# Kernel optimization log

Measured on AMD Instinct MI355X. Metric: run time of the kernel, lower is better.

The kernel has to match this reference:

```python
import jax, jax.numpy as jnp
import numpy as np

B, T_ENC, IN_SIZE = 512, 256, 32
HID, N_LAYERS, OUT_SIZE, PRED_W = 256, 2, 1, 30


def _lstm_layer(x, h0, c0, W_ih, W_hh, b_ih, b_hh):
    """x: [B,T,D]; PyTorch gate order i,f,g,o. Returns (ys [B,T,H], h, c)."""
    pre = jnp.einsum('btd,gd->btg', x, W_ih) + b_ih  # precompute input gates [B,T,4H]
    def step(carry, p):
        h, c = carry
        gates = p + h @ W_hh.T + b_hh
        i, f, g, o = jnp.split(gates, 4, axis=-1)
        c = jax.nn.sigmoid(f) * c + jax.nn.sigmoid(i) * jnp.tanh(g)
        h = jax.nn.sigmoid(o) * jnp.tanh(c)
        return (h, c), h
    (h, c), ys = jax.lax.scan(step, (h0, c0), jnp.swapaxes(pre, 0, 1))
    return jnp.swapaxes(ys, 0, 1), h, c


def _lstm_stack(x, layer_params, h0s, c0s):
    """layer_params: list of (W_ih, W_hh, b_ih, b_hh); h0s/c0s: [L,B,H]."""
    y = x
    hs, cs = [], []
    for l, (W_ih, W_hh, b_ih, b_hh) in enumerate(layer_params):
        y, h, c = _lstm_layer(y, h0s[l], c0s[l], W_ih, W_hh, b_ih, b_hh)
        hs.append(h)
        cs.append(c)
    return y, jnp.stack(hs), jnp.stack(cs)


def setup_inputs() -> dict:
    key = jax.random.key(0)
    ks = iter(jax.random.split(key, 32))
    k = 1.0 / np.sqrt(HID)
    u = lambda shape: jax.random.uniform(next(ks), shape, jnp.float32, -k, k)
    inp = {
        'input': jax.random.normal(next(ks), (B, T_ENC, IN_SIZE), jnp.float32),
        'target': jax.random.normal(next(ks), (B, PRED_W), jnp.float32),
    }
    # encoder LSTM: layer0 input IN_SIZE, layer1 input HID
    for l, d_in in enumerate([IN_SIZE, HID]):
        inp[f'enc_W_ih{l}'] = u((4 * HID, d_in))
        inp[f'enc_W_hh{l}'] = u((4 * HID, HID))
        inp[f'enc_b_ih{l}'] = u((4 * HID,))
        inp[f'enc_b_hh{l}'] = u((4 * HID,))
    # decoder LSTM: layer0 input OUT_SIZE(=1), layer1 input HID
    for l, d_in in enumerate([OUT_SIZE, HID]):
        inp[f'dec_W_ih{l}'] = u((4 * HID, d_in))
        inp[f'dec_W_hh{l}'] = u((4 * HID, HID))
        inp[f'dec_b_ih{l}'] = u((4 * HID,))
        inp[f'dec_b_hh{l}'] = u((4 * HID,))
    inp['fc_w'] = u((OUT_SIZE, HID))
    inp['fc_b'] = u((OUT_SIZE,))
    return inp


def reference(input, target,
              enc_W_ih0, enc_W_hh0, enc_b_ih0, enc_b_hh0,
              enc_W_ih1, enc_W_hh1, enc_b_ih1, enc_b_hh1,
              dec_W_ih0, dec_W_hh0, dec_b_ih0, dec_b_hh0,
              dec_W_ih1, dec_W_hh1, dec_b_ih1, dec_b_hh1,
              fc_w, fc_b):
    b = input.shape[0]
    enc_params = [(enc_W_ih0, enc_W_hh0, enc_b_ih0, enc_b_hh0),
                  (enc_W_ih1, enc_W_hh1, enc_b_ih1, enc_b_hh1)]
    dec_params = [(dec_W_ih0, dec_W_hh0, dec_b_ih0, dec_b_hh0),
                  (dec_W_ih1, dec_W_hh1, dec_b_ih1, dec_b_hh1)]
    z = jnp.zeros((N_LAYERS, b, HID), input.dtype)
    # encoder: discard outputs, keep final (hidden, cell)
    _, h, c = _lstm_stack(input, enc_params, z, z)
    # decoder with teacher_forcing_ratio=1.0: inputs are target[:, t] at each step
    dec_x = target[:, :, None]  # [B, PRED_W, 1]
    ys, _, _ = _lstm_stack(dec_x, dec_params, h, c)  # [B, PRED_W, HID]
    out = ys @ fc_w.T + fc_b  # [B, PRED_W, 1]
    return out[..., 0]  # squeeze(2) -> [B, PRED_W]
```

## Files before the change

kernel.cpp:

```cpp
#include <hip/hip_runtime.h>
#include <cmath>

#define NBLK 256
#define NTH  512
#define BATCH 512
#define TENC  256
#define INSZ  32
#define HID   256
#define PREDW 30
#define NTICKS 288

typedef __attribute__((ext_vector_type(4))) float f32x4;
typedef __attribute__((ext_vector_type(8))) short short8;
typedef __attribute__((ext_vector_type(8))) __bf16 bf16x8;
typedef __attribute__((ext_vector_type(4))) unsigned int u32x4;

struct SParams {
  const float *input, *target;
  const float *eWih0, *eWhh0, *eBih0, *eBhh0;
  const float *eWih1, *eWhh1, *eBih1, *eBhh1;
  const float *dWih0, *dWhh0, *dBih0, *dBhh0;
  const float *dWih1, *dWhh1, *dBih1, *dBhh1;
  const float *fcw, *fcb;
  float *out;
  char *h0img, *h1img;
  unsigned *cnt;
};

__device__ __forceinline__ float sigf(float x) { return 1.0f / (1.0f + expf(-x)); }

__device__ __forceinline__ unsigned short f2bf(float x) {
  unsigned u = __float_as_uint(x);
  u += 0x7fffu + ((u >> 16) & 1u);
  return (unsigned short)(u >> 16);
}
__device__ __forceinline__ float bf2f(unsigned short h) {
  return __uint_as_float(((unsigned)h) << 16);
}

__device__ __forceinline__ void gload_lds16(const void* g, void* l) {
  __builtin_amdgcn_global_load_lds(
      (const __attribute__((address_space(1))) unsigned int*)g,
      (__attribute__((address_space(3))) unsigned int*)l, 16, 0, 0);
}

__device__ __forceinline__ void gstore16_sc(void* gptr, u32x4 v) {
  asm volatile("global_store_dwordx4 %0, %1, off sc0 sc1" :: "v"(gptr), "v"(v) : "memory");
}
__device__ __forceinline__ void gstore4_sc(float* gptr, float v) {
  asm volatile("global_store_dword %0, %1, off sc0 sc1" :: "v"(gptr), "v"(v) : "memory");
}

__device__ __forceinline__ f32x4 mfma16(bf16x8 a, bf16x8 b, f32x4 c) {
  return __builtin_amdgcn_mfma_f32_16x16x32_bf16(a, b, c, 0, 0, 0);
}

__device__ __forceinline__ size_t imgoff(int par, int rt, int hl, int kt, int nt) {
  return (size_t)((((par * 8 + rt) * 2 + hl) * 8 + kt) * 4 + nt) * 1024;
}

__device__ __forceinline__ void grid_sync(unsigned* cnt, unsigned tgt) {
  asm volatile("s_waitcnt vmcnt(0)" ::: "memory");
  __syncthreads();
  if (threadIdx.x == 0) {
    __hip_atomic_fetch_add(cnt, 1u, __ATOMIC_RELAXED, __HIP_MEMORY_SCOPE_AGENT);
    while (__hip_atomic_load(cnt, __ATOMIC_RELAXED, __HIP_MEMORY_SCOPE_AGENT) < tgt) { }
    (void)__hip_atomic_load(cnt, __ATOMIC_ACQUIRE, __HIP_MEMORY_SCOPE_AGENT);
  }
  __syncthreads();
  asm volatile("" ::: "memory");
}

extern __shared__ char smem[];

__global__ __launch_bounds__(NTH) void seq2seq_kernel(SParams p)
{
  const int tid  = threadIdx.x;
  const int bid  = blockIdx.x;
  const int lane = tid & 63;
  const int wid  = tid >> 6;

  const int rtile = bid & 7;
  const int role  = bid >> 3;
  const int layer = role >> 4;
  const int dtile = role & 15;
  const int R0 = rtile * 64;
  const int D0 = dtile * 16;

  const int m    = wid >> 1;
  const int jj   = wid & 1;
  const int bl15 = lane & 15;
  const int dim_local = m * 4 + (lane >> 4);
  const int dim  = D0 + dim_local;

  const int KT_ih = layer ? 8 : 1;
  char* sWih = smem;
  char* sWhh = smem + (size_t)2 * 4 * KT_ih * 1024;
  char* ring = sWhh + 65536;
  char* xbuf = ring + 3 * 8192;
  unsigned* h_img = (unsigned*)ring;

  unsigned* mycnt = p.cnt + rtile * 64;

  const float *bi_e, *bh_e, *bi_d, *bh_d;
  if (layer == 0) { bi_e = p.eBih0; bh_e = p.eBhh0; bi_d = p.dBih0; bh_d = p.dBhh0; }
  else            { bi_e = p.eBih1; bh_e = p.eBhh1; bi_d = p.dBih1; bh_d = p.dBhh1; }
  float be[4], bd[4], wxd[4];
  #pragma unroll
  for (int g = 0; g < 4; ++g) {
    const int grow = g * HID + dim;
    be[g]  = bi_e[grow] + bh_e[grow];
    bd[g]  = bi_d[grow] + bh_d[grow];
    wxd[g] = (layer == 0) ? p.dWih0[grow] : 0.0f;
  }
  const float fcwj = p.fcw[dim];
  const float fcb0 = p.fcb[0];

  for (int idx = bid * NTH + tid; idx < BATCH * PREDW; idx += NBLK * NTH)
    gstore4_sc(p.out + idx, fcb0);

  auto convW = [&](const float* __restrict__ W, int K, char* dst) {
    const int lg8 = (K == 32) ? 2 : 5;
    const int K8  = 1 << lg8;
    const int KT  = K8 >> 2;
    for (int s = tid; s < 64 * K8; s += NTH) {
      const int r = s >> lg8, k8 = s & (K8 - 1);
      const float* src = W + (size_t)((r & 3) * HID + D0 + (r >> 2)) * K + k8 * 8;
      float4 v0 = *(const float4*)src;
      float4 v1 = *(const float4*)(src + 4);
      float v[8] = {v0.x, v0.y, v0.z, v0.w, v1.x, v1.y, v1.z, v1.w};
      short8 h8, l8;
      #pragma unroll
      for (int q = 0; q < 8; ++q) {
        unsigned short hq = f2bf(v[q]);
        h8[q] = (short)hq;
        l8[q] = (short)f2bf(v[q] - bf2f(hq));
      }
      const int mm = r >> 4, kt = k8 >> 2, li = (r & 15) | ((k8 & 3) << 4);
      *(short8*)(dst + (size_t)((0 * 4 + mm) * KT + kt) * 1024 + li * 16) = h8;
      *(short8*)(dst + (size_t)((1 * 4 + mm) * KT + kt) * 1024 + li * 16) = l8;
    }
  };
  if (layer == 0) { convW(p.eWih0, INSZ, sWih); convW(p.eWhh0, HID, sWhh); }
  else            { convW(p.eWih1, HID, sWih); convW(p.eWhh1, HID, sWhh); }
  __syncthreads();

  float c0 = 0.0f, c1 = 0.0f;
  unsigned epoch = 1;

  for (int t = 0; t < NTICKS; ++t) {
    const int rp = t & 1, wp = rp ^ 1;

    bool active = false, isdec = false;
    int s = 0;
    if (layer == 0) {
      if (t < 256)                 { active = true; }
      else if (t >= 257 && t < 287){ active = true; isdec = true; s = t - 257; }
    } else {
      if (t >= 1 && t <= 256)      { active = true; }
      else if (t >= 258)           { active = true; isdec = true; s = t - 258; }
    }
    const int nsteps = layer ? 16 : 8;

    if (active) {
      f32x4 a0, a1;
      #pragma unroll
      for (int q = 0; q < 4; ++q) {
        const float b = isdec ? bd[q] : be[q];
        a0[q] = b; a1[q] = b;
      }

      if (layer == 0 && !isdec) {
        if (tid < 256) {
          const int b = tid >> 2, k8 = tid & 3;
          const float* src = p.input + (size_t)(R0 + b) * TENC * INSZ + t * INSZ + k8 * 8;
          float4 v0 = *(const float4*)src;
          float4 v1 = *(const float4*)(src + 4);
          float v[8] = {v0.x, v0.y, v0.z, v0.w, v1.x, v1.y, v1.z, v1.w};
          short8 h8, l8;
          #pragma unroll
          for (int q = 0; q < 8; ++q) {
            unsigned short hq = f2bf(v[q]);
            h8[q] = (short)hq;
            l8[q] = (short)f2bf(v[q] - bf2f(hq));
          }
          const int li = (b & 15) | (k8 << 4), nt = b >> 4;
          *(short8*)(xbuf + (size_t)(0 * 4 + nt) * 1024 + li * 16) = h8;
          *(short8*)(xbuf + (size_t)(1 * 4 + nt) * 1024 + li * 16) = l8;
        }
        __syncthreads();
      }

      auto ringIssue = [&](int st, int slot) {
        const int hl = wid >> 2, nt = wid & 3;
        int kt; const char* base;
        if (layer == 0) { base = p.h0img; kt = st; }
        else { base = (st >= 8) ? p.h1img : p.h0img; kt = st & 7; }
        const char* g = base + imgoff(rp, rtile, hl, kt, nt) + (size_t)lane * 16;
        gload_lds16(g, ring + (size_t)slot * 8192 + (hl * 4 + nt) * 1024);
      };

      ringIssue(0, 0);
      ringIssue(1, 1);

      if (layer == 0 && !isdec) {
        bf16x8 ah = *(const bf16x8*)(sWih + (size_t)(0 * 4 + m) * 1024 + lane * 16);
        bf16x8 al = *(const bf16x8*)(sWih + (size_t)(1 * 4 + m) * 1024 + lane * 16);
        bf16x8 b0h = *(const bf16x8*)(xbuf + (size_t)(0 * 4 + 2 * jj + 0) * 1024 + lane * 16);
        bf16x8 b0l = *(const bf16x8*)(xbuf + (size_t)(1 * 4 + 2 * jj + 0) * 1024 + lane * 16);
        bf16x8 b1h = *(const bf16x8*)(xbuf + (size_t)(0 * 4 + 2 * jj + 1) * 1024 + lane * 16);
        bf16x8 b1l = *(const bf16x8*)(xbuf + (size_t)(1 * 4 + 2 * jj + 1) * 1024 + lane * 16);
        a0 = mfma16(ah, b0h, a0); a0 = mfma16(ah, b0l, a0); a0 = mfma16(al, b0h, a0);
        a1 = mfma16(ah, b1h, a1); a1 = mfma16(ah, b1l, a1); a1 = mfma16(al, b1h, a1);
      }

      for (int i = 0; i < nsteps; ++i) {
        if (i < nsteps - 1) asm volatile("s_waitcnt vmcnt(1)" ::: "memory");
        else                asm volatile("s_waitcnt vmcnt(0)" ::: "memory");
        __builtin_amdgcn_s_barrier();
        asm volatile("" ::: "memory");
        if (i + 2 < nsteps) ringIssue(i + 2, (i + 2) % 3);

        char* wreg; int kt;
        if (layer == 0) { wreg = sWhh; kt = i; }
        else            { wreg = (i < 8) ? sWih : sWhh; kt = i & 7; }
        char* sp = ring + (size_t)(i % 3) * 8192;
        bf16x8 ah = *(const bf16x8*)(wreg + (size_t)((0 * 4 + m) * 8 + kt) * 1024 + lane * 16);
        bf16x8 al = *(const bf16x8*)(wreg + (size_t)((1 * 4 + m) * 8 + kt) * 1024 + lane * 16);
        bf16x8 b0h = *(const bf16x8*)(sp + (size_t)(0 * 4 + 2 * jj + 0) * 1024 + lane * 16);
        bf16x8 b0l = *(const bf16x8*)(sp + (size_t)(1 * 4 + 2 * jj + 0) * 1024 + lane * 16);
        bf16x8 b1h = *(const bf16x8*)(sp + (size_t)(0 * 4 + 2 * jj + 1) * 1024 + lane * 16);
        bf16x8 b1l = *(const bf16x8*)(sp + (size_t)(1 * 4 + 2 * jj + 1) * 1024 + lane * 16);
        a0 = mfma16(ah, b0h, a0); a0 = mfma16(ah, b0l, a0); a0 = mfma16(al, b0h, a0);
        a1 = mfma16(ah, b1h, a1); a1 = mfma16(ah, b1l, a1); a1 = mfma16(al, b1h, a1);
      }
      __syncthreads();

      #pragma unroll
      for (int nt = 0; nt < 2; ++nt) {
        f32x4 a = nt ? a1 : a0;
        const int bg = R0 + (2 * jj + nt) * 16 + bl15;
        if (isdec && layer == 0) {
          const float xv = p.target[bg * PREDW + s];
          #pragma unroll
          for (int q = 0; q < 4; ++q) a[q] = fmaf(xv, wxd[q], a[q]);
        }
        const float ig = sigf(a[0]);
        const float fg = sigf(a[1]);
        const float gg = tanhf(a[2]);
        const float og = sigf(a[3]);
        float& cr = nt ? c1 : c0;
        cr = fg * cr + ig * gg;
        const float h = og * tanhf(cr);
        if (isdec && layer == 1) {
          float pp = fcwj * h;
          pp += __shfl_xor(pp, 16);
          pp += __shfl_xor(pp, 32);
          if (lane < 16) atomicAdd(p.out + bg * PREDW + s, pp);
        }
        const unsigned hi = f2bf(h);
        const unsigned lo = f2bf(h - bf2f((unsigned short)hi));
        h_img[dim_local * 65 + (2 * jj + nt) * 16 + bl15] = (hi << 16) | lo;
      }
      __syncthreads();

      if (tid < 256) {
        const int hl = tid >> 7, t2 = tid & 127;
        const int nt = t2 >> 5, lg = (t2 >> 4) & 1, bl = t2 & 15;
        unsigned w[4];
        #pragma unroll
        for (int q = 0; q < 4; ++q) {
          const unsigned v0 = h_img[(lg * 8 + 2 * q) * 65 + nt * 16 + bl];
          const unsigned v1 = h_img[(lg * 8 + 2 * q + 1) * 65 + nt * 16 + bl];
          w[q] = hl ? (((v1 & 0xffffu) << 16) | (v0 & 0xffffu))
                    : ((v1 & 0xffff0000u) | (v0 >> 16));
        }
        const int kg = ((dtile & 1) * 2) + lg, kt = dtile >> 1;
        char* base = layer ? p.h1img : p.h0img;
        u32x4 val; val.x = w[0]; val.y = w[1]; val.z = w[2]; val.w = w[3];
        gstore16_sc(base + imgoff(wp, rtile, hl, kt, nt) + (size_t)(bl | (kg << 4)) * 16, val);
      }
    } else if ((layer == 0 && t == 256) || (layer == 1 && t == 257)) {
      if (tid < 256) {
        const int hl = tid >> 7, t2 = tid & 127;
        const int nt = t2 >> 5, lg = (t2 >> 4) & 1, bl = t2 & 15;
        const int kg = ((dtile & 1) * 2) + lg, kt = dtile >> 1;
        char* base = layer ? p.h1img : p.h0img;
        const size_t sl = (size_t)(bl | (kg << 4)) * 16;
        u32x4 v = *(const u32x4*)(base + imgoff(rp, rtile, hl, kt, nt) + sl);
        gstore16_sc(base + imgoff(wp, rtile, hl, kt, nt) + sl, v);
      }
      __syncthreads();
      if (layer == 0) { convW(p.dWhh0, HID, sWhh); }
      else            { convW(p.dWih1, HID, sWih); convW(p.dWhh1, HID, sWhh); }
      __syncthreads();
    }

    grid_sync(mycnt, 32u * epoch);
    ++epoch;
  }
}

extern "C" void kernel_launch(void* const* d_in, const int* in_sizes, int n_in,
                              void* d_out, int out_size, void* d_ws, size_t ws_size,
                              hipStream_t stream)
{
  SParams p;
  p.input = (const float*)d_in[0];
  p.target = (const float*)d_in[1];
  p.eWih0 = (const float*)d_in[2];  p.eWhh0 = (const float*)d_in[3];
  p.eBih0 = (const float*)d_in[4];  p.eBhh0 = (const float*)d_in[5];
  p.eWih1 = (const float*)d_in[6];  p.eWhh1 = (const float*)d_in[7];
  p.eBih1 = (const float*)d_in[8];  p.eBhh1 = (const float*)d_in[9];
  p.dWih0 = (const float*)d_in[10]; p.dWhh0 = (const float*)d_in[11];
  p.dBih0 = (const float*)d_in[12]; p.dBhh0 = (const float*)d_in[13];
  p.dWih1 = (const float*)d_in[14]; p.dWhh1 = (const float*)d_in[15];
  p.dBih1 = (const float*)d_in[16]; p.dBhh1 = (const float*)d_in[17];
  p.fcw = (const float*)d_in[18];   p.fcb = (const float*)d_in[19];
  p.out = (float*)d_out;

  char* ws = (char*)d_ws;
  p.h0img = ws;
  p.h1img = ws + (1 << 20);
  p.cnt   = (unsigned*)(ws + (2 << 20));

  (void)hipMemsetAsync(d_ws, 0, (size_t)(2 << 20) + 2048, stream);

  const int shmem = 155648;
  (void)hipFuncSetAttribute((const void*)seq2seq_kernel,
                            hipFuncAttributeMaxDynamicSharedMemorySize, shmem);
  hipLaunchKernelGGL(seq2seq_kernel, dim3(NBLK), dim3(NTH), shmem, stream, p);
}
```

Baseline: 2.968 ms.

## Keep LSTM weights in registers and deepen the h-state LDS prefetch ring

Each thread now holds its split-bf16 weight fragments in registers (wh/wl arrays) instead of LDS, which removes two LDS reads per MFMA step and shrinks shared memory. The async global-to-LDS ring grows from 3 slots with prefetch distance 2 to 8 slots with distance 6, and the cache-coherence bits on those loads are set so the recurrent h images are read past stale caches. It also drops the acquire load in the grid barrier and adds a launch-bounds occupancy hint. This raises register pressure from 32 live bf16x8 values, and the weaker barrier ordering depends on the sc-bit loads for correctness.

```diff
diff --git a/kernel.cpp b/kernel.cpp
--- a/kernel.cpp
+++ b/kernel.cpp
@@ -38,10 +38,10 @@
   return __uint_as_float(((unsigned)h) << 16);
 }
 
-__device__ __forceinline__ void gload_lds16(const void* g, void* l) {
+__device__ __forceinline__ void gload_lds16_sc(const void* g, void* l) {
   __builtin_amdgcn_global_load_lds(
       (const __attribute__((address_space(1))) unsigned int*)g,
-      (__attribute__((address_space(3))) unsigned int*)l, 16, 0, 0);
+      (__attribute__((address_space(3))) unsigned int*)l, 16, 0, 17);
 }
 
 __device__ __forceinline__ void gstore16_sc(void* gptr, u32x4 v) {
@@ -57,6 +57,17 @@
 
 __device__ __forceinline__ size_t imgoff(int par, int rt, int hl, int kt, int nt) {
   return (size_t)((((par * 8 + rt) * 2 + hl) * 8 + kt) * 4 + nt) * 1024;
+}
+
+__device__ __forceinline__ void wait_vmcnt_k(int k) {
+  switch (k) {
+    case 0: asm volatile("s_waitcnt vmcnt(0)" ::: "memory"); break;
+    case 1: asm volatile("s_waitcnt vmcnt(1)" ::: "memory"); break;
+    case 2: asm volatile("s_waitcnt vmcnt(2)" ::: "memory"); break;
+    case 3: asm volatile("s_waitcnt vmcnt(3)" ::: "memory"); break;
+    case 4: asm volatile("s_waitcnt vmcnt(4)" ::: "memory"); break;
+    default: asm volatile("s_waitcnt vmcnt(5)" ::: "memory"); break;
+  }
 }
 
 __device__ __forceinline__ void grid_sync(unsigned* cnt, unsigned tgt) {
@@ -65,7 +76,6 @@
   if (threadIdx.x == 0) {
     __hip_atomic_fetch_add(cnt, 1u, __ATOMIC_RELAXED, __HIP_MEMORY_SCOPE_AGENT);
     while (__hip_atomic_load(cnt, __ATOMIC_RELAXED, __HIP_MEMORY_SCOPE_AGENT) < tgt) { }
-    (void)__hip_atomic_load(cnt, __ATOMIC_ACQUIRE, __HIP_MEMORY_SCOPE_AGENT);
   }
   __syncthreads();
   asm volatile("" ::: "memory");
@@ -73,7 +83,7 @@
 
 extern __shared__ char smem[];
 
-__global__ __launch_bounds__(NTH) void seq2seq_kernel(SParams p)
+__global__ __launch_bounds__(NTH, 2) void seq2seq_kernel(SParams p)
 {
   const int tid  = threadIdx.x;
   const int bid  = blockIdx.x;
@@ -90,15 +100,13 @@
   const int m    = wid >> 1;
   const int jj   = wid & 1;
   const int bl15 = lane & 15;
+  const int k8l  = lane >> 4;
   const int dim_local = m * 4 + (lane >> 4);
   const int dim  = D0 + dim_local;
 
-  const int KT_ih = layer ? 8 : 1;
-  char* sWih = smem;
-  char* sWhh = smem + (size_t)2 * 4 * KT_ih * 1024;
-  char* ring = sWhh + 65536;
-  char* xbuf = ring + 3 * 8192;
-  unsigned* h_img = (unsigned*)ring;
+  char* ring = smem;
+  char* xbuf = smem + 8 * 8192;
+  unsigned* h_img = (unsigned*)smem;
 
   unsigned* mycnt = p.cnt + rtile * 64;
 
@@ -119,31 +127,34 @@
   for (int idx = bid * NTH + tid; idx < BATCH * PREDW; idx += NBLK * NTH)
     gstore4_sc(p.out + idx, fcb0);
 
-  auto convW = [&](const float* __restrict__ W, int K, char* dst) {
-    const int lg8 = (K == 32) ? 2 : 5;
-    const int K8  = 1 << lg8;
-    const int KT  = K8 >> 2;
-    for (int s = tid; s < 64 * K8; s += NTH) {
-      const int r = s >> lg8, k8 = s & (K8 - 1);
-      const float* src = W + (size_t)((r & 3) * HID + D0 + (r >> 2)) * K + k8 * 8;
-      float4 v0 = *(const float4*)src;
-      float4 v1 = *(const float4*)(src + 4);
-      float v[8] = {v0.x, v0.y, v0.z, v0.w, v1.x, v1.y, v1.z, v1.w};
-      short8 h8, l8;
-      #pragma unroll
-      for (int q = 0; q < 8; ++q) {
-        unsigned short hq = f2bf(v[q]);
-        h8[q] = (short)hq;
-        l8[q] = (short)f2bf(v[q] - bf2f(hq));
-      }
-      const int mm = r >> 4, kt = k8 >> 2, li = (r & 15) | ((k8 & 3) << 4);
-      *(short8*)(dst + (size_t)((0 * 4 + mm) * KT + kt) * 1024 + li * 16) = h8;
-      *(short8*)(dst + (size_t)((1 * 4 + mm) * KT + kt) * 1024 + li * 16) = l8;
+  const int wrow = (bl15 & 3) * HID + D0 + m * 4 + (bl15 >> 2);
+  auto convReg = [&](const float* __restrict__ W, int K, int kt, bf16x8& hf, bf16x8& lf) {
+    const float* src = W + (size_t)wrow * K + (size_t)(kt * 4 + k8l) * 8;
+    float4 v0 = *(const float4*)src;
+    float4 v1 = *(const float4*)(src + 4);
+    float v[8] = {v0.x, v0.y, v0.z, v0.w, v1.x, v1.y, v1.z, v1.w};
+    short8 hs, ls;
+    #pragma unroll
+    for (int e = 0; e < 8; ++e) {
+      unsigned short hq = f2bf(v[e]);
+      hs[e] = (short)hq;
+      ls[e] = (short)f2bf(v[e] - bf2f(hq));
     }
+    hf = __builtin_bit_cast(bf16x8, hs);
+    lf = __builtin_bit_cast(bf16x8, ls);
   };
-  if (layer == 0) { convW(p.eWih0, INSZ, sWih); convW(p.eWhh0, HID, sWhh); }
-  else            { convW(p.eWih1, HID, sWih); convW(p.eWhh1, HID, sWhh); }
-  __syncthreads();
+
+  bf16x8 wh[16], wl[16];
+  if (layer == 0) {
+    convReg(p.eWih0, INSZ, 0, wh[0], wl[0]);
+    #pragma unroll
+    for (int kt = 0; kt < 8; ++kt) convReg(p.eWhh0, HID, kt, wh[1 + kt], wl[1 + kt]);
+  } else {
+    #pragma unroll
+    for (int kt = 0; kt < 8; ++kt) convReg(p.eWih1, HID, kt, wh[kt], wl[kt]);
+    #pragma unroll
+    for (int kt = 0; kt < 8; ++kt) convReg(p.eWhh1, HID, kt, wh[8 + kt], wl[8 + kt]);
+  }
 
   float c0 = 0.0f, c1 = 0.0f;
   unsigned epoch = 1;
@@ -160,7 +171,6 @@
       if (t >= 1 && t <= 256)      { active = true; }
       else if (t >= 258)           { active = true; isdec = true; s = t - 258; }
     }
-    const int nsteps = layer ? 16 : 8;
 
     if (active) {
       f32x4 a0, a1;
@@ -169,6 +179,15 @@
         const float b = isdec ? bd[q] : be[q];
         a0[q] = b; a1[q] = b;
       }
+
+      auto ringIssue = [&](int st, int slot) {
+        const int hl = wid >> 2, nt = wid & 3;
+        const char* base; int kt;
+        if (layer == 0) { base = p.h0img; kt = st; }
+        else { base = (st >= 8) ? p.h1img : p.h0img; kt = st & 7; }
+        const char* g = base + imgoff(rp, rtile, hl, kt, nt) + (size_t)lane * 16;
+        gload_lds16_sc(g, ring + (size_t)slot * 8192 + (hl * 4 + nt) * 1024);
+      };
 
       if (layer == 0 && !isdec) {
         if (tid < 256) {
@@ -188,51 +207,41 @@
           *(short8*)(xbuf + (size_t)(0 * 4 + nt) * 1024 + li * 16) = h8;
           *(short8*)(xbuf + (size_t)(1 * 4 + nt) * 1024 + li * 16) = l8;
         }
+      }
+
+      #pragma unroll
+      for (int st = 0; st < 6; ++st) ringIssue(st, st);
+
+      if (layer == 0 && !isdec) {
         __syncthreads();
-      }
-
-      auto ringIssue = [&](int st, int slot) {
-        const int hl = wid >> 2, nt = wid & 3;
-        int kt; const char* base;
-        if (layer == 0) { base = p.h0img; kt = st; }
-        else { base = (st >= 8) ? p.h1img : p.h0img; kt = st & 7; }
-        const char* g = base + imgoff(rp, rtile, hl, kt, nt) + (size_t)lane * 16;
-        gload_lds16(g, ring + (size_t)slot * 8192 + (hl * 4 + nt) * 1024);
-      };
-
-      ringIssue(0, 0);
-      ringIssue(1, 1);
-
-      if (layer == 0 && !isdec) {
-        bf16x8 ah = *(const bf16x8*)(sWih + (size_t)(0 * 4 + m) * 1024 + lane * 16);
-        bf16x8 al = *(const bf16x8*)(sWih + (size_t)(1 * 4 + m) * 1024 + lane * 16);
-        bf16x8 b0h = *(const bf16x8*)(xbuf + (size_t)(0 * 4 + 2 * jj + 0) * 1024 + lane * 16);
-        bf16x8 b0l = *(const bf16x8*)(xbuf + (size_t)(1 * 4 + 2 * jj + 0) * 1024 + lane * 16);
-        bf16x8 b1h = *(const bf16x8*)(xbuf + (size_t)(0 * 4 + 2 * jj + 1) * 1024 + lane * 16);
-        bf16x8 b1l = *(const bf16x8*)(xbuf + (size_t)(1 * 4 + 2 * jj + 1) * 1024 + lane * 16);
+        bf16x8 b0h = *(const bf16x8*)(xbuf + (size_t)(0 + 2 * jj + 0) * 1024 + lane * 16);
+        bf16x8 b0l = *(const bf16x8*)(xbuf + (size_t)(4 + 2 * jj + 0) * 1024 + lane * 16);
+        bf16x8 b1h = *(const bf16x8*)(xbuf + (size_t)(0 + 2 * jj + 1) * 1024 + lane * 16);
+        bf16x8 b1l = *(const bf16x8*)(xbuf + (size_t)(4 + 2 * jj + 1) * 1024 + lane * 16);
+        a0 = mfma16(wh[0], b0h, a0); a0 = mfma16(wh[0], b0l, a0); a0 = mfma16(wl[0], b0h, a0);
+        a1 = mfma16(wh[0], b1h, a1); a1 = mfma16(wh[0], b1l, a1); a1 = mfma16(wl[0], b1h, a1);
+      }
+
+      auto ringStep = [&](int i, int NS, bf16x8 ah, bf16x8 al) {
+        const int kk = NS - 1 - i;
+        wait_vmcnt_k(kk < 5 ? kk : 5);
+        __builtin_amdgcn_s_barrier();
+        asm volatile("" ::: "memory");
+        if (i + 6 < NS) ringIssue(i + 6, (i + 6) & 7);
+        char* sp = ring + (size_t)(i & 7) * 8192;
+        bf16x8 b0h = *(const bf16x8*)(sp + (size_t)(0 + 2 * jj + 0) * 1024 + lane * 16);
+        bf16x8 b0l = *(const bf16x8*)(sp + (size_t)(4 + 2 * jj + 0) * 1024 + lane * 16);
+        bf16x8 b1h = *(const bf16x8*)(sp + (size_t)(0 + 2 * jj + 1) * 1024 + lane * 16);
+        bf16x8 b1l = *(const bf16x8*)(sp + (size_t)(4 + 2 * jj + 1) * 1024 + lane * 16);
         a0 = mfma16(ah, b0h, a0); a0 = mfma16(ah, b0l, a0); a0 = mfma16(al, b0h, a0);
         a1 = mfma16(ah, b1h, a1); a1 = mfma16(ah, b1l, a1); a1 = mfma16(al, b1h, a1);
-      }
-
-      for (int i = 0; i < nsteps; ++i) {
-        if (i < nsteps - 1) asm volatile("s_waitcnt vmcnt(1)" ::: "memory");
-        else                asm volatile("s_waitcnt vmcnt(0)" ::: "memory");
-        __builtin_amdgcn_s_barrier();
-        asm volatile("" ::: "memory");
-        if (i + 2 < nsteps) ringIssue(i + 2, (i + 2) % 3);
-
-        char* wreg; int kt;
-        if (layer == 0) { wreg = sWhh; kt = i; }
-        else            { wreg = (i < 8) ? sWih : sWhh; kt = i & 7; }
-        char* sp = ring + (size_t)(i % 3) * 8192;
-        bf16x8 ah = *(const bf16x8*)(wreg + (size_t)((0 * 4 + m) * 8 + kt) * 1024 + lane * 16);
-        bf16x8 al = *(const bf16x8*)(wreg + (size_t)((1 * 4 + m) * 8 + kt) * 1024 + lane * 16);
-        bf16x8 b0h = *(const bf16x8*)(sp + (size_t)(0 * 4 + 2 * jj + 0) * 1024 + lane * 16);
-        bf16x8 b0l = *(const bf16x8*)(sp + (size_t)(1 * 4 + 2 * jj + 0) * 1024 + lane * 16);
-        bf16x8 b1h = *(const bf16x8*)(sp + (size_t)(0 * 4 + 2 * jj + 1) * 1024 + lane * 16);
-        bf16x8 b1l = *(const bf16x8*)(sp + (size_t)(1 * 4 + 2 * jj + 1) * 1024 + lane * 16);
-        a0 = mfma16(ah, b0h, a0); a0 = mfma16(ah, b0l, a0); a0 = mfma16(al, b0h, a0);
-        a1 = mfma16(ah, b1h, a1); a1 = mfma16(ah, b1l, a1); a1 = mfma16(al, b1h, a1);
+      };
+      if (layer == 0) {
+        #pragma unroll
+        for (int i = 0; i < 8; ++i) ringStep(i, 8, wh[1 + i], wl[1 + i]);
+      } else {
+        #pragma unroll
+        for (int i = 0; i < 16; ++i) ringStep(i, 16, wh[i], wl[i]);
       }
       __syncthreads();
 
@@ -290,10 +299,15 @@
         u32x4 v = *(const u32x4*)(base + imgoff(rp, rtile, hl, kt, nt) + sl);
         gstore16_sc(base + imgoff(wp, rtile, hl, kt, nt) + sl, v);
       }
-      __syncthreads();
-      if (layer == 0) { convW(p.dWhh0, HID, sWhh); }
-      else            { convW(p.dWih1, HID, sWih); convW(p.dWhh1, HID, sWhh); }
-      __syncthreads();
+      if (layer == 0) {
+        #pragma unroll
+        for (int kt = 0; kt < 8; ++kt) convReg(p.dWhh0, HID, kt, wh[1 + kt], wl[1 + kt]);
+      } else {
+        #pragma unroll
+        for (int kt = 0; kt < 8; ++kt) convReg(p.dWih1, HID, kt, wh[kt], wl[kt]);
+        #pragma unroll
+        for (int kt = 0; kt < 8; ++kt) convReg(p.dWhh1, HID, kt, wh[8 + kt], wl[8 + kt]);
+      }
     }
 
     grid_sync(mycnt, 32u * epoch);
@@ -326,7 +340,7 @@
 
   (void)hipMemsetAsync(d_ws, 0, (size_t)(2 << 20) + 2048, stream);
 
-  const int shmem = 155648;
+  const int shmem = 8 * 8192 + 8192;
   (void)hipFuncSetAttribute((const void*)seq2seq_kernel,
                             hipFuncAttributeMaxDynamicSharedMemorySize, shmem);
   hipLaunchKernelGGL(seq2seq_kernel, dim3(NBLK), dim3(NTH), shmem, stream, p);
```

After: 2.756 ms. 7.1% less time.
